# Kernel tuning notes

Measured on AMD Instinct MI355X. Metric: run time of the kernel, lower is better.

## Reference

```python
import jax, jax.numpy as jnp
import numpy as np

C = 32           # in_channels
KH, KW = 3, 3    # kernel_range
SHIFT = 1
NP = KH * KW


def conv2d(x, w, b, pad):
    # x: NCHW, w: OIHW
    y = jax.lax.conv_general_dilated(
        x, w, window_strides=(1, 1), padding=[(pad, pad), (pad, pad)],
        dimension_numbers=('NCHW', 'OIHW', 'NCHW'))
    return y + b[None, :, None, None]


def setup_inputs() -> dict:
    key = jax.random.key(0)
    ks = jax.random.split(key, 14)
    p = lambda k, shape: (jax.random.normal(k, shape, dtype=jnp.float32) * 0.02)
    inp = {
        'x':  jax.random.normal(ks[0], (4, C, 256, 256), dtype=jnp.float32),
        'wk': p(ks[1], (C * NP, C, 1, 1)), 'bk': p(ks[2], (C * NP,)),
        'wv': p(ks[3], (C * NP, C, 1, 1)), 'bv': p(ks[4], (C * NP,)),
        'wq': p(ks[5], (C, C, 1, 1)),      'bq': p(ks[6], (C,)),
        'w1': p(ks[7], (C, C, 3, 3)),      'b1': p(ks[8], (C,)),
        'w2': p(ks[9], (2 * C, C, 3, 3)),  'b2': p(ks[10], (2 * C,)),
        'w3': p(ks[11], (C, 2 * C, 3, 3)), 'b3': p(ks[12], (C,)),
    }
    return inp


def reference(x, wk, bk, wv, bv, wq, bq, w1, b1, w2, b2, w3, b3):
    B, D, H, W = x.shape
    h_half, w_half = KH // 2, KW // 2
    ph, pw = h_half * SHIFT, w_half * SHIFT

    x_k = conv2d(x, wk, bk, 0)  # (B, D*NP, H, W)
    x_v = conv2d(x, wv, bv, 0)
    x_q = conv2d(x, wq, bq, 0)  # (B, D, H, W)

    pad4 = ((0, 0), (0, 0), (ph, ph), (pw, pw))
    x_k = jnp.pad(x_k, pad4)
    x_v = jnp.pad(x_v, pad4)
    mask_pad = jnp.pad(jnp.ones((B, 1, H, W), x.dtype), pad4)

    k_ls, v_ls, m_ls = [], [], []
    layer = 0
    for i in range(-h_half, h_half + 1):
        for j in range(-w_half, w_half + 1):
            r0 = ph + i * SHIFT
            c0 = pw + j * SHIFT
            k_ls.append(x_k[:, layer * D:(layer + 1) * D, r0:r0 + H, c0:c0 + W])
            v_ls.append(x_v[:, layer * D:(layer + 1) * D, r0:r0 + H, c0:c0 + W])
            m_ls.append(mask_pad[:, :, r0:r0 + H, c0:c0 + W])
            layer += 1

    # Faithful to torch .view semantics: flat row-major reshape, NOT a permute.
    k = jnp.stack(k_ls, axis=1).reshape(B * H * W, NP, D)   # (B,NP,D,H,W) -> flat
    v = jnp.stack(v_ls, axis=1).reshape(B * H * W, NP, D)
    m = jnp.stack(m_ls, axis=1).reshape(B * H * W, NP, 1)
    q = x_q.reshape(B * H * W, 1, D)                         # (B,D,H,W) -> flat

    scores = jnp.matmul(k, jnp.swapaxes(q, -1, -2)) * m / 8.0  # (N, NP, 1)
    alpha = jax.nn.softmax(scores, axis=1)
    res = jnp.matmul(jnp.swapaxes(alpha, -1, -2), v)           # (N, 1, D)
    t = res.reshape(B, D, H, W)

    t = jax.nn.relu(conv2d(t, w1, b1, 1))
    t = jax.nn.relu(conv2d(t, w2, b2, 1))
    t = jax.nn.relu(conv2d(t, w3, b3, 1))
    return t
```

## Files before the change

kernel.cpp:

```cpp
#include <hip/hip_runtime.h>
#include <hip/hip_bf16.h>

#define B_ 4
#define C_ 32
#define H_ 256
#define W_ 256
#define S_ 65536
#define NP_ 9
#define OC_ 288
#define PR 258
#define PWN 264
#define XGUARD 260
#define XSTRIDE 66056

using bf16 = __hip_bfloat16;
typedef __attribute__((ext_vector_type(8)))  short  short8;
typedef __attribute__((ext_vector_type(4)))  short  short4_t;
typedef __attribute__((ext_vector_type(16))) float  f32x16;

__device__ __forceinline__ float b2f(short s) {
    return __uint_as_float(((unsigned)(unsigned short)s) << 16);
}

template<int IC, int OC>
__device__ __forceinline__ void prepA_body(int fid, const float* __restrict__ w,
                                           bf16* __restrict__ apk)
{
    constexpr int NK = 9 * IC / 16;
    int tile = fid >> 9;
    int l = (fid >> 3) & 63;
    int j = fid & 7;
    int mt = tile / NK;
    int ks = tile - mt * NK;
    int q = l >> 5;
    int oc = mt * 32 + (l & 31);
    int k = ks * 16 + q * 8 + j;
    int tap = k / IC;
    int ic = k - tap * IC;
    apk[fid] = __float2bfloat16(w[((oc * IC + ic) * 3 + tap / 3) * 3 + tap % 3]);
}

template<int G>
__device__ __forceinline__ void zerob_body(int b, int p, uint4* __restrict__ buf)
{
    int gran;
    if (p < 2 * PWN * G) {
        int row = (p < PWN * G) ? 0 : 257;
        int rem = p % (PWN * G);
        gran = row * PWN * G + rem;
    } else {
        int p2 = p - 2 * PWN * G;
        int col = (p2 < 256 * G) ? 0 : 257;
        int rem = p2 % (256 * G);
        int r = rem / G + 1;
        int icg = rem - (rem / G) * G;
        gran = (r * PWN + col) * G + icg;
    }
    buf[(size_t)b * PR * PWN * G + gran] = uint4{0, 0, 0, 0};
}

__global__ __launch_bounds__(256) void k_prep(
    const float* __restrict__ wk, const float* __restrict__ wv,
    const float* __restrict__ wq,
    const float* __restrict__ w1, const float* __restrict__ w2,
    const float* __restrict__ w3,
    bf16* __restrict__ apk0, bf16* __restrict__ apk1,
    bf16* __restrict__ apk2, bf16* __restrict__ apk3,
    uint4* __restrict__ tA, uint4* __restrict__ t1, uint4* __restrict__ t2,
    uint4* __restrict__ xb16)
{
    int idx = blockIdx.x * 256 + threadIdx.x;
    if (idx < 19456) {
        int j    = idx & 7;
        int lane = (idx >> 3) & 63;
        int ks   = (idx >> 9) & 1;
        int mt   = idx >> 10;
        int oc = lane & 31;
        int ic = ks * 16 + (lane >> 5) * 8 + j;
        const float* w; int ocg;
        if (mt < 9)       { w = wk; ocg = mt * 32 + oc; }
        else if (mt < 18) { w = wv; ocg = (mt - 9) * 32 + oc; }
        else              { w = wq; ocg = oc; }
        apk0[idx] = __float2bfloat16(w[ocg * C_ + ic]);
    } else if (idx < 28672) {
        prepA_body<32, 32>(idx - 19456, w1, apk1);
    } else if (idx < 47104) {
        prepA_body<32, 64>(idx - 28672, w2, apk2);
    } else if (idx < 65536) {
        prepA_body<64, 32>(idx - 47104, w3, apk3);
    } else if (idx < 82176) {
        int i5 = idx - 65536;
        zerob_body<4>(i5 / 4160, i5 % 4160, tA);
    } else if (idx < 98816) {
        int i6 = idx - 82176;
        zerob_body<4>(i6 / 4160, i6 % 4160, t1);
    } else if (idx < 132096) {
        int i7 = idx - 98816;
        zerob_body<8>(i7 / 8320, i7 % 8320, t2);
    } else if (idx < 142464) {
        int i8 = idx - 132096;
        size_t off;
        if (i8 < 8320) {
            int b = i8 / 2080, r = i8 - b * 2080;
            if (r < 1040) off = (size_t)b * (XSTRIDE * 4) + r;
            else          off = ((size_t)b * XSTRIDE + XGUARD + 65536) * 4 + (r - 1040);
        } else {
            off = (size_t)(4 * XSTRIDE) * 4 + (i8 - 8320);
        }
        xb16[off] = uint4{0, 0, 0, 0};
    }
}

__global__ __launch_bounds__(256) void k_q(
    const float* __restrict__ x, const bf16* __restrict__ apk,
    const float* __restrict__ bq, bf16* __restrict__ xqs, bf16* __restrict__ xb16)
{
    __shared__ bf16 lbuf[32][140];
    int bh  = blockIdx.x >> 9;
    int blk = blockIdx.x & 511;
    int pixw0 = blk << 7;
    int tid  = threadIdx.x;
    int wvi  = tid >> 6;
    int lane = tid & 63;
    int col  = lane & 31, q = lane >> 5;
    int pix  = pixw0 + wvi * 32 + col;

    const float* xb = x + (size_t)bh * (C_ * S_);

    short8 bfrag[2];
#pragma unroll
    for (int kk = 0; kk < 2; ++kk)
#pragma unroll
        for (int j = 0; j < 8; ++j) {
            bf16 h = __float2bfloat16(xb[(size_t)(kk * 16 + q * 8 + j) * S_ + pix]);
            bfrag[kk][j] = *reinterpret_cast<short*>(&h);
        }

    {
        bf16* xr = xb16 + ((size_t)bh * XSTRIDE + XGUARD + pix) * 32;
        *reinterpret_cast<short8*>(xr + (q << 3))       = bfrag[0];
        *reinterpret_cast<short8*>(xr + ((2 + q) << 3)) = bfrag[1];
    }

    const short8* apkv = reinterpret_cast<const short8*>(apk);
    f32x16 acc = {};
    acc = __builtin_amdgcn_mfma_f32_32x32x16_bf16(bfrag[0], apkv[(18 * 2 + 0) * 64 + lane], acc, 0, 0, 0);
    acc = __builtin_amdgcn_mfma_f32_32x32x16_bf16(bfrag[1], apkv[(18 * 2 + 1) * 64 + lane], acc, 0, 0, 0);
    float bbv = bq[col];
#pragma unroll
    for (int g4 = 0; g4 < 4; ++g4) {
        short4_t sv;
#pragma unroll
        for (int j = 0; j < 4; ++j) {
            bf16 hb = __float2bfloat16(acc[g4 * 4 + j] + bbv);
            sv[j] = *reinterpret_cast<short*>(&hb);
        }
        *reinterpret_cast<short4_t*>(&lbuf[col][wvi * 32 + 8 * g4 + 4 * q]) = sv;
    }
    __syncthreads();
    int ch0 = tid >> 4, chk = tid & 15, ch1 = ch0 + 16;
    short8 v0 = *reinterpret_cast<const short8*>(&lbuf[ch0][chk * 8]);
    short8 v1 = *reinterpret_cast<const short8*>(&lbuf[ch1][chk * 8]);
    int tb = (pixw0 >> 5) + (chk >> 2);
    int G2 = chk & 3;
    bf16* qb = xqs + (size_t)bh * (32 * S_);
    short4_t lo0 = {v0[0], v0[1], v0[2], v0[3]}, hi0 = {v0[4], v0[5], v0[6], v0[7]};
    short4_t lo1 = {v1[0], v1[1], v1[2], v1[3]}, hi1 = {v1[4], v1[5], v1[6], v1[7]};
    *reinterpret_cast<short4_t*>(qb + (ch0 * 2048 + tb) * 32 + G2 * 4)      = lo0;
    *reinterpret_cast<short4_t*>(qb + (ch0 * 2048 + tb) * 32 + 16 + G2 * 4) = hi0;
    *reinterpret_cast<short4_t*>(qb + (ch1 * 2048 + tb) * 32 + G2 * 4)      = lo1;
    *reinterpret_cast<short4_t*>(qb + (ch1 * 2048 + tb) * 32 + 16 + G2 * 4) = hi1;
}


#define DO_TILE(T, SQ)                                                                \
{                                                                                     \
    int Tg = tgbase + (T);                                                            \
    if (Tg < 2048) {                                                                  \
        unsigned n = (unsigned)plane_base + ((unsigned)Tg << 5);                      \
        unsigned tl = n / 288u;                                                       \
        const bf16* qp = xqb + ((size_t)tl << 5) + (q << 4);                          \
        short8 qA = *reinterpret_cast<const short8*>(qp);                             \
        short8 qB = *reinterpret_cast<const short8*>(qp + 8);                         \
        int xib = ((T) << 5) + 257 + shf + col;                                       \
        int swx = (xib ^ (xib >> 2)) & 3;                                             \
        short8 fa = *reinterpret_cast<const short8*>(&xs[xib * 4 + (q ^ swx)]);       \
        short8 fb = *reinterpret_cast<const short8*>(&xs[xib * 4 + ((2 + q) ^ swx)]); \
        bool hbad  = ((((T) << 5) < hb_lo) || (((T) << 5) >= hb_hi));                 \
        bool tb_lo = (dj == -1) && ((Tg & 7) == 0);                                   \
        bool tb_hi = (dj == 1) && ((Tg & 7) == 7);                                    \
        if (tb_lo && q == 0) qA[0] = 0;                                               \
        if (tb_hi && q == 1) qB[7] = 0;                                               \
        f32x16 ka = {bK, bK, bK, bK, bK, bK, bK, bK, bK, bK, bK, bK, bK, bK, bK, bK}; \
        ka = __builtin_amdgcn_mfma_f32_32x32x16_bf16(fa, apkv[(p * 2 + 0) * 64 + lane], ka, 0, 0, 0); \
        ka = __builtin_amdgcn_mfma_f32_32x32x16_bf16(fb, apkv[(p * 2 + 1) * 64 + lane], ka, 0, 0, 0); \
        float dot = 0.f;                                                              \
        _Pragma("unroll")                                                             \
        for (int j3 = 0; j3 < 4; ++j3) {                                              \
            dot += ka[j3]      * b2f(qA[j3]);                                         \
            dot += ka[4 + j3]  * b2f(qA[4 + j3]);                                     \
            dot += ka[8 + j3]  * b2f(qB[j3]);                                         \
            dot += ka[12 + j3] * b2f(qB[4 + j3]);                                     \
        }                                                                             \
        if (hbad) dot = 0.f;                                                          \
        dot += __shfl_xor(dot, 32);                                                   \
        if (q == (SQ)) scL[(T) * 32 + col] = dot;                                     \
        f32x16 vh = {bV, bV, bV, bV, bV, bV, bV, bV, bV, bV, bV, bV, bV, bV, bV, bV}; \
        vh = __builtin_amdgcn_mfma_f32_32x32x16_bf16(fa, apkv[((9 + p) * 2 + 0) * 64 + lane], vh, 0, 0, 0); \
        vh = __builtin_amdgcn_mfma_f32_32x32x16_bf16(fb, apkv[((9 + p) * 2 + 1) * 64 + lane], vh, 0, 0, 0); \
        _Pragma("unroll")                                                             \
        for (int G2 = 0; G2 < 4; ++G2) {                                              \
            short4_t sv;                                                              \
            _Pragma("unroll")                                                         \
            for (int j3 = 0; j3 < 4; ++j3) {                                          \
                float val = hbad ? 0.f : vh[G2 * 4 + j3];                             \
                bf16 hcv = __float2bfloat16(val);                                     \
                sv[j3] = *reinterpret_cast<short*>(&hcv);                             \
            }                                                                         \
            if (G2 == 0 && tb_lo && q == 0) sv[0] = 0;                                \
            if (G2 == 3 && tb_hi && q == 1) sv[3] = 0;                                \
            *reinterpret_cast<short4_t*>(kvB + col * 1616 +                           \
                ((((T) << 2) + (G2 ^ xcol)) << 4) + q * 8) = sv;                      \
        }                                                                             \
    }                                                                                 \
}

__global__ __launch_bounds__(1024, 4) void k_fused(
    const bf16* __restrict__ xb16,
    const bf16* __restrict__ apk,
    const float* __restrict__ bk, const float* __restrict__ bv,
    const bf16* __restrict__ xqs,
    bf16* __restrict__ att)
{
    extern __shared__ char smem_raw[];
    uint4* xs  = reinterpret_cast<uint4*>(smem_raw);
    char*  kvB = smem_raw + 84096;
    float* scL = reinterpret_cast<float*>(smem_raw + 135808);
    unsigned short* scM = reinterpret_cast<unsigned short*>(smem_raw + 139008);

    int bb = blockIdx.x >> 7;
    int s0 = (blockIdx.x & 127) << 9;
    int tgbase = s0 >> 5;

    int tid  = threadIdx.x;
    int lane = tid & 63;
    int wv   = tid >> 6;
    int col  = lane & 31;
    int q    = lane >> 5;
    int xcol = (col >> 3) & 3;

    size_t qbase = ((size_t)bb << 21);
    const bf16* xqb = xqs + qbase;
    const short8* apkv = reinterpret_cast<const short8*>(apk);

    {
        const uint4* src = reinterpret_cast<const uint4*>(xb16) +
                           ((size_t)bb * XSTRIDE + XGUARD + s0 - 257) * 4;
        for (int i = tid; i < 5256; i += 1024) {
            int xi = i >> 2, g = i & 3;
            int sw = (xi ^ (xi >> 2)) & 3;
            xs[xi * 4 + (g ^ sw)] = src[i];
        }
    }

    if (tid < 576) {
        int krow = tid >= 288;
        int i2 = tid - (krow ? 288 : 0);
        int pp = i2 >> 5, dpc = i2 & 31;
        int plane_base_r = ((pp << 5) + dpc) << 16;
        unsigned tl = ((unsigned)(plane_base_r + s0 + 287)) / 288u + (unsigned)krow;
        int sk0 = (int)(tl * 288u) - plane_base_r;
        unsigned m = 0;
        if (sk0 < s0 + 512 && sk0 <= 65248) {
            m = 0x8000u;
#pragma unroll
            for (int seg = 0; seg < 9; ++seg) {
                int rm = (int)tl * 9 + seg;
                int pm = rm >> 16, sm = rm & 65535;
                int dim = pm / 3 - 1, djm = pm - (pm / 3) * 3 - 1;
                int hm = sm >> 8, wm = sm & 255;
                bool mval = ((unsigned)(hm + dim) < 256u) && ((unsigned)(wm + djm) < 256u);
                m |= (mval ? 1u : 0u) << seg;
            }
        }
        scM[tid] = (unsigned short)m;
    }
    __syncthreads();

    int grp  = tid >> 3, sub = tid & 7;
    int dp   = grp & 31;
    int krow = (grp >> 5) & 1;
    int hh   = sub >> 1;
    int sh   = sub & 1;
    bool athr = tid < 512;
    int swz = (dp >> 3) & 3;

#pragma unroll 1
    for (int p = 0; p < 9; ++p) {
        int di = p / 3 - 1, dj = p - (p / 3) * 3 - 1;
        int shf = di * 256 + dj;
        int hb_lo = (di == -1) ? (256 - s0) : (-0x40000000);
        int hb_hi = (di == 1) ? (65280 - s0) : 0x40000000;
        float bK = bk[p * 32 + col];
        float bV = bv[p * 32 + col];
        int plane_base = ((p << 5) + col) << 16;

        DO_TILE(wv, 0)
        if (wv < 9) { DO_TILE(wv + 16, 1) }
        __syncthreads();

        if (athr) {
            unsigned mflags = scM[krow * 288 + p * 32 + dp];
            if (mflags & 0x8000u) {
                int plane_base_r = ((p << 5) + dp) << 16;
                unsigned tl = ((unsigned)(plane_base_r + s0 + 287)) / 288u + (unsigned)krow;
                int sk0 = (int)(tl * 288u) - plane_base_r;
                int t0 = (sk0 - s0) >> 5;
                float sc[9];
#pragma unroll
                for (int seg = 0; seg < 9; ++seg)
                    sc[seg] = ((mflags >> seg) & 1u) ? scL[(t0 + seg) * 32 + dp] * 0.125f : 0.f;
                float mx = sc[0];
#pragma unroll
                for (int s2 = 1; s2 < 9; ++s2) mx = fmaxf(mx, sc[s2]);
                float wgt[9];
                float sum = 0.f;
#pragma unroll
                for (int s2 = 0; s2 < 9; ++s2) { wgt[s2] = __expf(sc[s2] - mx); sum += wgt[s2]; }
                float inv_ = 1.f / sum;

                float oacc[4] = {0.f, 0.f, 0.f, 0.f};
#pragma unroll
                for (int seg = 0; seg < 9; ++seg) {
                    short4_t vg = *reinterpret_cast<const short4_t*>(
                        kvB + dp * 1616 + ((((t0 + seg) << 2) + (hh ^ swz)) << 4) + sh * 8);
                    float w_ = wgt[seg];
#pragma unroll
                    for (int j = 0; j < 4; ++j) oacc[j] += w_ * b2f(vg[j]);
                }
                short4_t sv;
#pragma unroll
                for (int j = 0; j < 4; ++j) {
                    bf16 h = __float2bfloat16(oacc[j] * inv_);
                    sv[j] = *reinterpret_cast<short*>(&h);
                }
                *reinterpret_cast<short4_t*>(att + qbase + ((size_t)tl << 5) + hh * 8 + sh * 4) = sv;
            }
        }
        __syncthreads();
    }
}

__global__ __launch_bounds__(320) void k_strad(
    const float* __restrict__ x,
    const float* __restrict__ wk, const float* __restrict__ bk,
    const float* __restrict__ wv, const float* __restrict__ bv,
    const bf16* __restrict__ xqs, bf16* __restrict__ att)
{
    __shared__ float kL[288], vL[288], qL[32], wgtL[10];
    int e = blockIdx.x;
    int b = e >> 8, i = e & 255;
    int g = i >> 3, u = i & 7;
    int tl = g * 2048 + (((2040 + u) * 1593) & 2047);
    int tid = threadIdx.x;

    if (tid < 288) {
        int f  = tl * 288 + tid;
        int cp = f >> 16;
        int sp = f & 65535;
        int tap = cp >> 5;
        int di = tap / 3 - 1, dj = tap - (tap / 3) * 3 - 1;
        int h = sp >> 8, w = sp & 255;
        bool valid = ((unsigned)(h + di) < 256u) && ((unsigned)(w + dj) < 256u);
        float kv_ = 0.f, vv_ = 0.f;
        if (valid) {
            int sx = sp + di * 256 + dj;
            const float* xp = x + (size_t)b * (C_ * S_) + sx;
            float ks = bk[cp], vs = bv[cp];
#pragma unroll
            for (int ic = 0; ic < 32; ++ic) {
                float xv_ = xp[(size_t)ic * S_];
                ks += wk[cp * 32 + ic] * xv_;
                vs += wv[cp * 32 + ic] * xv_;
            }
            kv_ = ks; vv_ = vs;
        }
        kL[tid] = kv_; vL[tid] = vv_;
    }
    if (tid < 32) {
        int pos = ((tid >> 2) & 1) * 16 + (tid >> 3) * 4 + (tid & 3);
        bf16 hv = xqs[(size_t)b * (32 * S_) + (size_t)tl * 32 + pos];
        qL[tid] = b2f(*reinterpret_cast<short*>(&hv));
    }
    __syncthreads();
    if (tid < 9) {
        float dot = 0.f;
#pragma unroll
        for (int d = 0; d < 32; ++d) dot += kL[tid * 32 + d] * qL[d];
        int rm = tl * 9 + tid;
        int pm = rm >> 16, sm = rm & 65535;
        int dim = pm / 3 - 1, djm = pm - (pm / 3) * 3 - 1;
        int hm = sm >> 8, wm = sm & 255;
        bool mval = ((unsigned)(hm + dim) < 256u) && ((unsigned)(wm + djm) < 256u);
        wgtL[tid] = mval ? dot * 0.125f : 0.f;
    }
    __syncthreads();
    if (tid == 0) {
        float mx = wgtL[0];
#pragma unroll
        for (int s2 = 1; s2 < 9; ++s2) mx = fmaxf(mx, wgtL[s2]);
        float sum = 0.f;
#pragma unroll
        for (int s2 = 0; s2 < 9; ++s2) { wgtL[s2] = __expf(wgtL[s2] - mx); sum += wgtL[s2]; }
        wgtL[9] = 1.f / sum;
    }
    __syncthreads();
    if (tid < 32) {
        float acc = 0.f;
#pragma unroll
        for (int seg = 0; seg < 9; ++seg) acc += wgtL[seg] * vL[seg * 32 + tid];
        att[(size_t)b * 2097152 + (size_t)tl * 32 + tid] = __float2bfloat16(acc * wgtL[9]);
    }
}

__global__ __launch_bounds__(256) void k_repack(
    const bf16* __restrict__ att, bf16* __restrict__ tA)
{
    int idx = blockIdx.x * 256 + threadIdx.x;
    int icg = idx & 3;
    int ps  = idx >> 2;
    int b = ps >> 16;
    int s = ps & 65535;
    const bf16* src = att + (size_t)b * (32 * S_) + icg * 8 * S_ + s;
    short8 v;
#pragma unroll
    for (int j = 0; j < 8; ++j)
        v[j] = *reinterpret_cast<const short*>(src + (size_t)j * S_);
    int row = (s >> 8) + 1, colp = (s & 255) + 1;
    *reinterpret_cast<short8*>(tA + ((size_t)((b * PR + row) * PWN + colp)) * 32 + icg * 8) = v;
}

template<int IC, int OC, bool NCHW_OUT>
__global__ __launch_bounds__(256) void k_conv3s(
    const bf16* __restrict__ in,
    const bf16* __restrict__ apk,
    const float* __restrict__ bs,
    void* __restrict__ outv)
{
    constexpr int G    = IC / 8;
    constexpr int M    = OC / 32;
    constexpr int KPT  = IC / 16;
    constexpr int NK   = 9 * KPT;
    constexpr int NT   = 2;
    constexpr int ROWP = 66;
    constexpr int ROWG = ROWP * G;
    constexpr int TOTG = 6 * ROWG;

    __shared__ uint4 smem[TOTG];

    int wg   = blockIdx.x;
    int orig = (wg & 7) * 128 + (wg >> 3);
    int b   = orig >> 8;
    int rem = orig & 255;
    int h0  = (rem >> 2) << 2;
    int w0  = (rem & 3) * 64;

    int tid = threadIdx.x;

    {
        const uint4* src = reinterpret_cast<const uint4*>(in);
#pragma unroll
        for (int i = 0; i < (TOTG + 255) / 256; ++i) {
            int idx = tid + i * 256;
            if (idx < TOTG) {
                int dr = idx / ROWG;
                int r2 = idx - dr * ROWG;
                uint4 v = src[((size_t)(b * PR + h0 + dr) * PWN + w0) * G + r2];
                int px = r2 >> ((G == 4) ? 2 : 3);
                int sw = (G == 4) ? ((px ^ (px >> 2)) & 3) : (px & 7);
                smem[dr * ROWG + (r2 & ~(G - 1)) + ((r2 ^ sw) & (G - 1))] = v;
            }
        }
    }
    __syncthreads();

    int lane = tid & 63;
    int wid  = tid >> 6;
    int col  = lane & 31, q = lane >> 5;
    int h    = h0 + wid;

    const short8* apkv = reinterpret_cast<const short8*>(apk);

    f32x16 acc[NT][M];
#pragma unroll
    for (int nt = 0; nt < NT; ++nt)
#pragma unroll
        for (int mt = 0; mt < M; ++mt) acc[nt][mt] = (f32x16){};

#pragma unroll
    for (int tap = 0; tap < 9; ++tap) {
        int dr = tap / 3 + wid;
        int dj = tap % 3;
#pragma unroll
        for (int icq = 0; icq < KPT; ++icq) {
            short8 bfr[NT];
#pragma unroll
            for (int nt = 0; nt < NT; ++nt) {
                int px = nt * 32 + col + dj;
                int sw = (G == 4) ? ((px ^ (px >> 2)) & 3) : (px & 7);
                bfr[nt] = *reinterpret_cast<const short8*>(
                    &smem[dr * ROWG + px * G + ((icq * 2 + q) ^ sw)]);
            }
#pragma unroll
            for (int mt = 0; mt < M; ++mt) {
                short8 afr = apkv[(mt * NK + tap * KPT + icq) * 64 + lane];
#pragma unroll
                for (int nt = 0; nt < NT; ++nt)
                    acc[nt][mt] = __builtin_amdgcn_mfma_f32_32x32x16_bf16(
                        afr, bfr[nt], acc[nt][mt], 0, 0, 0);
            }
        }
    }

#pragma unroll
    for (int nt = 0; nt < NT; ++nt) {
        int wout = w0 + nt * 32 + col;
#pragma unroll
        for (int mt = 0; mt < M; ++mt) {
            if (NCHW_OUT) {
                float* out = (float*)outv;
#pragma unroll
                for (int r = 0; r < 16; ++r) {
                    int oc = mt * 32 + (r & 3) + 8 * (r >> 2) + 4 * q;
                    out[(size_t)((b * OC + oc) * H_ + h) * W_ + wout] =
                        fmaxf(acc[nt][mt][r] + bs[oc], 0.f);
                }
            } else {
                bf16* out = (bf16*)outv;
                size_t base = (size_t)((b * PR + h + 1) * PWN + wout + 1) * OC + mt * 32 + 4 * q;
#pragma unroll
                for (int g4 = 0; g4 < 4; ++g4) {
                    short4_t sv;
#pragma unroll
                    for (int r4 = 0; r4 < 4; ++r4) {
                        int oc = mt * 32 + 8 * g4 + 4 * q + r4;
                        bf16 hh = __float2bfloat16(fmaxf(acc[nt][mt][g4 * 4 + r4] + bs[oc], 0.f));
                        sv[r4] = *reinterpret_cast<short*>(&hh);
                    }
                    *reinterpret_cast<short4_t*>(out + base + 8 * g4) = sv;
                }
            }
        }
    }
}

extern "C" void kernel_launch(void* const* d_in, const int* in_sizes, int n_in,
                              void* d_out, int out_size, void* d_ws, size_t ws_size,
                              hipStream_t stream)
{
    const float* x  = (const float*)d_in[0];
    const float* wk = (const float*)d_in[1];
    const float* bk = (const float*)d_in[2];
    const float* wv = (const float*)d_in[3];
    const float* bv = (const float*)d_in[4];
    const float* wq = (const float*)d_in[5];
    const float* bq = (const float*)d_in[6];
    const float* w1 = (const float*)d_in[7];
    const float* b1 = (const float*)d_in[8];
    const float* w2 = (const float*)d_in[9];
    const float* b2 = (const float*)d_in[10];
    const float* w3 = (const float*)d_in[11];
    const float* b3 = (const float*)d_in[12];
    float* out = (float*)d_out;
    char* ws = (char*)d_ws;

    bf16* xqs  = (bf16*)(ws);
    bf16* tA   = (bf16*)(ws + 16777216);
    bf16* t1   = (bf16*)(ws + 34213888);
    bf16* t2   = (bf16*)(ws + 51650560);
    bf16* apk0 = (bf16*)(ws + 86523904);
    bf16* apk1 = (bf16*)(ws + 86562816);
    bf16* apk2 = (bf16*)(ws + 86581248);
    bf16* apk3 = (bf16*)(ws + 86618112);
    bf16* xb16 = (bf16*)(ws + 86654976);
    bf16* attB = (bf16*)d_out;

    static bool attr_set = false;
    if (!attr_set) {
        hipFuncSetAttribute(reinterpret_cast<const void*>(k_fused),
                            hipFuncAttributeMaxDynamicSharedMemorySize, 140160);
        attr_set = true;
    }

    k_prep<<<557, 256, 0, stream>>>(wk, wv, wq, w1, w2, w3,
                                    apk0, apk1, apk2, apk3,
                                    (uint4*)tA, (uint4*)t1, (uint4*)t2, (uint4*)xb16);

    k_q<<<2048, 256, 0, stream>>>(x, apk0, bq, xqs, xb16);

    k_fused<<<512, 1024, 140160, stream>>>(xb16, apk0, bk, bv, xqs, attB);

    k_strad<<<1024, 320, 0, stream>>>(x, wk, bk, wv, bv, xqs, attB);

    k_repack<<<4096, 256, 0, stream>>>(attB, tA);

    k_conv3s<32, 32, false><<<1024, 256, 0, stream>>>(tA, apk1, b1, (void*)t1);
    k_conv3s<32, 64, false><<<1024, 256, 0, stream>>>(t1, apk2, b2, (void*)t2);
    k_conv3s<64, 32, true ><<<1024, 256, 0, stream>>>(t2, apk3, b3, (void*)out);
}
```

Before: 168.4 us.

## Spread attention epilogue over all threads and read bf16 NHWC input in straddle kernel

The softmax-weighted V reduction in the fused kernel now runs on all 1024 threads, each producing two channels, instead of 512 threads producing four. The straddle kernel now reads the guarded bf16 channel-last copy of x with vector loads instead of strided fp32 reads across channel planes. The hbad zeroing of the score dot product is removed. The risk is that the straddle kernel's numerics change from fp32 to bf16 input, and dropping the hbad mask relies on the mask flags already covering those positions.

```diff
diff --git a/kernel.cpp b/kernel.cpp
--- a/kernel.cpp
+++ b/kernel.cpp
@@ -16,6 +16,7 @@
 using bf16 = __hip_bfloat16;
 typedef __attribute__((ext_vector_type(8)))  short  short8;
 typedef __attribute__((ext_vector_type(4)))  short  short4_t;
+typedef __attribute__((ext_vector_type(2)))  short  short2_t;
 typedef __attribute__((ext_vector_type(16))) float  f32x16;
 
 __device__ __forceinline__ float b2f(short s) {
@@ -202,7 +203,6 @@
             dot += ka[8 + j3]  * b2f(qB[j3]);                                         \
             dot += ka[12 + j3] * b2f(qB[4 + j3]);                                     \
         }                                                                             \
-        if (hbad) dot = 0.f;                                                          \
         dot += __shfl_xor(dot, 32);                                                   \
         if (q == (SQ)) scL[(T) * 32 + col] = dot;                                     \
         f32x16 vh = {bV, bV, bV, bV, bV, bV, bV, bV, bV, bV, bV, bV, bV, bV, bV, bV}; \
@@ -287,13 +287,12 @@
     }
     __syncthreads();
 
-    int grp  = tid >> 3, sub = tid & 7;
-    int dp   = grp & 31;
-    int krow = (grp >> 5) & 1;
-    int hh   = sub >> 1;
-    int sh   = sub & 1;
-    bool athr = tid < 512;
-    int swz = (dp >> 3) & 3;
+    int sub   = tid & 15;
+    int strip = tid >> 4;
+    int dp    = strip & 31;
+    int krow  = strip >> 5;
+    int swz   = (dp >> 3) & 3;
+    int vboff = dp * 1616 + (((sub >> 2) ^ swz) << 4) + ((sub >> 1) & 1) * 8 + (sub & 1) * 4;
 
 #pragma unroll 1
     for (int p = 0; p < 9; ++p) {
@@ -309,7 +308,7 @@
         if (wv < 9) { DO_TILE(wv + 16, 1) }
         __syncthreads();
 
-        if (athr) {
+        {
             unsigned mflags = scM[krow * 288 + p * 32 + dp];
             if (mflags & 0x8000u) {
                 int plane_base_r = ((p << 5) + dp) << 16;
@@ -329,22 +328,19 @@
                 for (int s2 = 0; s2 < 9; ++s2) { wgt[s2] = __expf(sc[s2] - mx); sum += wgt[s2]; }
                 float inv_ = 1.f / sum;
 
-                float oacc[4] = {0.f, 0.f, 0.f, 0.f};
+                const char* vb = kvB + vboff + t0 * 64;
+                float o0 = 0.f, o1 = 0.f;
 #pragma unroll
                 for (int seg = 0; seg < 9; ++seg) {
-                    short4_t vg = *reinterpret_cast<const short4_t*>(
-                        kvB + dp * 1616 + ((((t0 + seg) << 2) + (hh ^ swz)) << 4) + sh * 8);
+                    short2_t vg = *reinterpret_cast<const short2_t*>(vb + seg * 64);
                     float w_ = wgt[seg];
-#pragma unroll
-                    for (int j = 0; j < 4; ++j) oacc[j] += w_ * b2f(vg[j]);
+                    o0 += w_ * b2f(vg[0]);
+                    o1 += w_ * b2f(vg[1]);
                 }
-                short4_t sv;
-#pragma unroll
-                for (int j = 0; j < 4; ++j) {
-                    bf16 h = __float2bfloat16(oacc[j] * inv_);
-                    sv[j] = *reinterpret_cast<short*>(&h);
-                }
-                *reinterpret_cast<short4_t*>(att + qbase + ((size_t)tl << 5) + hh * 8 + sh * 4) = sv;
+                bf16 h0 = __float2bfloat16(o0 * inv_);
+                bf16 h1 = __float2bfloat16(o1 * inv_);
+                short2_t s2v = {*reinterpret_cast<short*>(&h0), *reinterpret_cast<short*>(&h1)};
+                *reinterpret_cast<short2_t*>(att + qbase + ((size_t)tl << 5) + sub * 2) = s2v;
             }
         }
         __syncthreads();
@@ -352,7 +348,7 @@
 }
 
 __global__ __launch_bounds__(320) void k_strad(
-    const float* __restrict__ x,
+    const bf16* __restrict__ xb16,
     const float* __restrict__ wk, const float* __restrict__ bk,
     const float* __restrict__ wv, const float* __restrict__ bv,
     const bf16* __restrict__ xqs, bf16* __restrict__ att)
@@ -375,14 +371,22 @@
         float kv_ = 0.f, vv_ = 0.f;
         if (valid) {
             int sx = sp + di * 256 + dj;
-            const float* xp = x + (size_t)b * (C_ * S_) + sx;
+            const bf16* xp = xb16 + ((size_t)b * XSTRIDE + XGUARD + sx) * 32;
+            const float* wkp = wk + cp * 32;
+            const float* wvp = wv + cp * 32;
             float ks = bk[cp], vs = bv[cp];
-#pragma unroll
-            for (int ic = 0; ic < 32; ++ic) {
-                float xv_ = xp[(size_t)ic * S_];
-                ks += wk[cp * 32 + ic] * xv_;
-                vs += wv[cp * 32 + ic] * xv_;
-            }
+            short8 xg[4];
+#pragma unroll
+            for (int gg = 0; gg < 4; ++gg)
+                xg[gg] = *reinterpret_cast<const short8*>(xp + gg * 8);
+#pragma unroll
+            for (int gg = 0; gg < 4; ++gg)
+#pragma unroll
+                for (int j = 0; j < 8; ++j) {
+                    float xv_ = b2f(xg[gg][j]);
+                    ks += wkp[gg * 8 + j] * xv_;
+                    vs += wvp[gg * 8 + j] * xv_;
+                }
             kv_ = ks; vv_ = vs;
         }
         kL[tid] = kv_; vL[tid] = vv_;
@@ -600,7 +604,7 @@
 
     k_fused<<<512, 1024, 140160, stream>>>(xb16, apk0, bk, bv, xqs, attB);
 
-    k_strad<<<1024, 320, 0, stream>>>(x, wk, bk, wv, bv, xqs, attB);
+    k_strad<<<1024, 320, 0, stream>>>(xb16, wk, bk, wv, bv, xqs, attB);
 
     k_repack<<<4096, 256, 0, stream>>>(attB, tA);
 
```

Result: no change. 168.9 us (+0.3%).
